# Performance work log

Measured on AMD Instinct MI355X. Metric: run time of the kernel, lower is better.

Reference implementation:

```python
import jax, jax.numpy as jnp
import numpy as np

IN_FEATURES = 4096
OUT_FEATURES = 4096
CODESZ = 8
CODEBOOK_SIZE = 256


def fwht(x):
    """Normalized fast Walsh-Hadamard transform over the last dim (power of 2).
    Equivalent to x @ (H / sqrt(n)); H symmetric so this serves both
    matmul_hadUt and matmul_hadU in the power-of-2 case (had=None, K=1)."""
    orig_shape = x.shape
    n = orig_shape[-1]
    x = x.reshape(-1, n)
    h = 2
    while h <= n:
        x = x.reshape(-1, n // h, 2, h // 2)
        a, b = x[..., 0, :], x[..., 1, :]
        x = jnp.stack([a + b, a - b], axis=-2)
        h *= 2
    x = x.reshape(orig_shape)
    return x * (1.0 / np.sqrt(n)).astype(np.float32)


def setup_inputs() -> dict:
    key = jax.random.key(0)
    k1, k2, k3, k4, k5, k6 = jax.random.split(key, 6)
    x = jax.random.normal(k1, (4, 2048, IN_FEATURES), dtype=jnp.float32)
    Qidxs = jax.random.randint(k2, (OUT_FEATURES, IN_FEATURES // CODESZ), 0, CODEBOOK_SIZE, dtype=jnp.int32)
    grid = jax.random.normal(k3, (CODEBOOK_SIZE, CODESZ), dtype=jnp.float32)
    SU = jax.random.uniform(k4, (IN_FEATURES,), dtype=jnp.float32)
    SV = jax.random.uniform(k5, (OUT_FEATURES,), dtype=jnp.float32)
    bias = jax.random.normal(k6, (OUT_FEATURES,), dtype=jnp.float32)
    return {"x": x, "Qidxs": Qidxs, "grid": grid, "SU": SU, "SV": SV, "bias": bias}


def reference(x, Qidxs, grid, SU, SV, bias):
    lead = x.shape[:-1]
    h = x.reshape(-1, IN_FEATURES)            # [T, in]
    h = h * SU                                 # scale by SU
    h = fwht(h)                                # matmul_hadUt (input rotation)
    # codebook dequant: gather code vectors and form W_hat [out, in]
    W_hat = grid[Qidxs].reshape(OUT_FEATURES, IN_FEATURES)
    y = h @ W_hat.T                            # [T, out]
    y = fwht(y)[:, :OUT_FEATURES]              # matmul_hadU (output rotation)
    y = y * SV
    y = y.reshape(*lead, OUT_FEATURES) + bias
    return y
```

## Files before the change

kernel.cpp:

```cpp
#include <hip/hip_runtime.h>

#define IN_F 4096
#define OUT_F 4096
#define NROWS 8192
#define BK 32
#define NT (IN_F / BK)

typedef __attribute__((ext_vector_type(4))) float f32x4;
typedef __attribute__((ext_vector_type(8))) short bf16x8;
typedef __attribute__((ext_vector_type(8))) unsigned short u16x8;

__device__ __forceinline__ unsigned short f2bf(float f) {
  union { float f; unsigned u; } x; x.f = f;
  unsigned r = x.u + 0x7FFFu + ((x.u >> 16) & 1u);
  return (unsigned short)(r >> 16);
}

__device__ __forceinline__ void gload_lds16(const unsigned short* g, unsigned short* l) {
  __builtin_amdgcn_global_load_lds((__attribute__((address_space(1))) void*)g,
                                   (__attribute__((address_space(3))) void*)l,
                                   16, 0, 0);
}

__device__ __forceinline__ void bfly16(float v[16]) {
#pragma unroll
  for (int s = 1; s < 16; s <<= 1) {
#pragma unroll
    for (int i = 0; i < 16; ++i) {
      if (!(i & s)) { float a = v[i], b = v[i + s]; v[i] = a + b; v[i + s] = a - b; }
    }
  }
}

__global__ __launch_bounds__(256) void dequant_kernel(const int* __restrict__ Q,
                                                      const float* __restrict__ grid,
                                                      unsigned short* __restrict__ Wb) {
  int g = blockIdx.x * 256 + threadIdx.x;
  int idx = Q[g];
  const f32x4* gp = (const f32x4*)(grid + idx * 8);
  f32x4 v0 = gp[0], v1 = gp[1];
  u16x8 o;
  o[0] = f2bf(v0[0]); o[1] = f2bf(v0[1]); o[2] = f2bf(v0[2]); o[3] = f2bf(v0[3]);
  o[4] = f2bf(v1[0]); o[5] = f2bf(v1[1]); o[6] = f2bf(v1[2]); o[7] = f2bf(v1[3]);
  *(u16x8*)(Wb + (size_t)g * 8) = o;
}

__global__ __launch_bounds__(256) void fwht1_kernel(const float* __restrict__ x,
                                                    const float* __restrict__ SU,
                                                    unsigned short* __restrict__ Hb) {
  __shared__ float buf[4096];
  int tid = threadIdx.x;
  size_t rbase = (size_t)blockIdx.x * IN_F;
  const f32x4* x4 = (const f32x4*)(x + rbase);
  const f32x4* su4 = (const f32x4*)SU;
  f32x4* b4 = (f32x4*)buf;
#pragma unroll
  for (int s = 0; s < 4; ++s) {
    int c = tid + 256 * s;
    f32x4 v = x4[c];
    f32x4 u = su4[c];
    v.x *= u.x; v.y *= u.y; v.z *= u.z; v.w *= u.w;
    b4[c] = v;
  }
  __syncthreads();
  float v[16];
  {
#pragma unroll
    for (int j = 0; j < 4; ++j) {
      f32x4 t4 = b4[tid * 4 + j];
      v[j*4+0] = t4.x; v[j*4+1] = t4.y; v[j*4+2] = t4.z; v[j*4+3] = t4.w;
    }
    bfly16(v);
#pragma unroll
    for (int j = 0; j < 4; ++j) {
      f32x4 t4; t4.x = v[j*4+0]; t4.y = v[j*4+1]; t4.z = v[j*4+2]; t4.w = v[j*4+3];
      b4[tid * 4 + j] = t4;
    }
  }
  __syncthreads();
  {
    int lo = tid & 15, hi = tid >> 4;
    int base = lo + (hi << 8);
#pragma unroll
    for (int j = 0; j < 16; ++j) v[j] = buf[base + (j << 4)];
    bfly16(v);
#pragma unroll
    for (int j = 0; j < 16; ++j) buf[base + (j << 4)] = v[j];
  }
  __syncthreads();
  {
#pragma unroll
    for (int j = 0; j < 16; ++j) v[j] = buf[tid + (j << 8)];
    bfly16(v);
#pragma unroll
    for (int j = 0; j < 16; ++j)
      Hb[rbase + tid + (j << 8)] = f2bf(v[j] * 0.015625f);
  }
}

__global__ __launch_bounds__(512) void gemm256_kernel(const unsigned short* __restrict__ Hb,
                                                      const unsigned short* __restrict__ Wb,
                                                      float* __restrict__ Y) {
  __shared__ unsigned short lds[4][2][256 * BK];
  const int tid = threadIdx.x;
  const int lane = tid & 63;
  const int wid = tid >> 6;
  const int wr = wid >> 2;
  const int wc = wid & 3;
  const int lrow = lane & 15;
  const int kgrp = lane >> 4;

  const int bid = blockIdx.x;
  const int swz = (bid & 7) * 64 + (bid >> 3);
  const int brow = (swz >> 4) << 8;
  const int bcol = (swz & 15) << 8;

  const int r0 = tid >> 2;
  const int sc = ((tid & 3) ^ ((r0 >> 1) & 3)) << 3;
  const unsigned short* AgR0 = Hb + (size_t)(brow + r0) * IN_F + sc;
  const unsigned short* AgR1 = Hb + (size_t)(brow + r0 + 128) * IN_F + sc;
  const unsigned short* BgR0 = Wb + (size_t)(bcol + r0) * IN_F + sc;
  const unsigned short* BgR1 = Wb + (size_t)(bcol + r0 + 128) * IN_F + sc;

#define STAGE(t) { \
  gload_lds16(AgR0 + (t) * BK, &lds[(t) & 3][0][tid * 8]); \
  gload_lds16(AgR1 + (t) * BK, &lds[(t) & 3][0][(tid + 512) * 8]); \
  gload_lds16(BgR0 + (t) * BK, &lds[(t) & 3][1][tid * 8]); \
  gload_lds16(BgR1 + (t) * BK, &lds[(t) & 3][1][(tid + 512) * 8]); }

  auto fragLd = [&](const unsigned short* base, int R) -> bf16x8 {
    return *(const bf16x8*)(base + R * BK + ((kgrp ^ ((R >> 1) & 3)) << 3));
  };

  const int ar = wr * 128 + lrow;
  const int br = wc * 64 + lrow;

#define READ_A(t, aS) { const unsigned short* As_ = &lds[(t) & 3][0][0]; \
  aS[0] = fragLd(As_, ar +   0); aS[1] = fragLd(As_, ar +  16); \
  aS[2] = fragLd(As_, ar +  32); aS[3] = fragLd(As_, ar +  48); \
  aS[4] = fragLd(As_, ar +  64); aS[5] = fragLd(As_, ar +  80); \
  aS[6] = fragLd(As_, ar +  96); aS[7] = fragLd(As_, ar + 112); }
#define READ_B(t) { const unsigned short* Bs_ = &lds[(t) & 3][1][0]; \
  b0 = fragLd(Bs_, br +  0); b1 = fragLd(Bs_, br + 16); \
  b2 = fragLd(Bs_, br + 32); b3 = fragLd(Bs_, br + 48); }

#define MM(i, A, B) acc[i] = __builtin_amdgcn_mfma_f32_16x16x32_bf16(A, B, acc[i], 0, 0, 0)
#define MMROW(m, aS) { \
  MM((m)*4+0, aS[m], b0); MM((m)*4+1, aS[m], b1); \
  MM((m)*4+2, aS[m], b2); MM((m)*4+3, aS[m], b3); }

#define TILE_BODY(t, aCur, aNxt) { \
  if ((t) + 3 <= NT) { asm volatile("s_waitcnt vmcnt(4)" ::: "memory"); } \
  else               { asm volatile("s_waitcnt vmcnt(0)" ::: "memory"); } \
  __builtin_amdgcn_s_barrier(); \
  if ((t) + 3 < NT) STAGE((t) + 3); \
  READ_B(t); \
  asm volatile("s_waitcnt lgkmcnt(0)" ::: "memory"); \
  __builtin_amdgcn_sched_barrier(0); \
  __builtin_amdgcn_s_setprio(1); \
  MMROW(0, aCur); MMROW(1, aCur); \
  __builtin_amdgcn_s_setprio(0); \
  if ((t) + 1 < NT) READ_A((t) + 1, aNxt); \
  __builtin_amdgcn_sched_barrier(0); \
  __builtin_amdgcn_s_setprio(1); \
  MMROW(2, aCur); MMROW(3, aCur); MMROW(4, aCur); MMROW(5, aCur); \
  MMROW(6, aCur); MMROW(7, aCur); \
  __builtin_amdgcn_s_setprio(0); }

  f32x4 acc[32] = {};
  bf16x8 aC[8], aN[8], b0, b1, b2, b3;

  STAGE(0); STAGE(1); STAGE(2);
  asm volatile("s_waitcnt vmcnt(4)" ::: "memory");
  __builtin_amdgcn_s_barrier();
  READ_A(0, aC);

  for (int t = 0; t < NT; t += 2) {
    TILE_BODY(t,     aC, aN);
    TILE_BODY(t + 1, aN, aC);
  }

#pragma unroll
  for (int mf = 0; mf < 8; ++mf) {
    int grow = brow + wr * 128 + mf * 16 + kgrp * 4;
    float* yp = Y + (size_t)grow * OUT_F + bcol + wc * 64 + lrow;
#pragma unroll
    for (int r = 0; r < 4; ++r)
#pragma unroll
      for (int nf = 0; nf < 4; ++nf)
        yp[(size_t)r * OUT_F + nf * 16] = acc[mf * 4 + nf][r];
  }
#undef STAGE
#undef READ_A
#undef READ_B
#undef MM
#undef MMROW
#undef TILE_BODY
}

__global__ __launch_bounds__(256) void fwht2_kernel(float* __restrict__ Y,
                                                    const float* __restrict__ SV,
                                                    const float* __restrict__ bias) {
  __shared__ float buf[4096];
  int tid = threadIdx.x;
  size_t rbase = (size_t)blockIdx.x * OUT_F;
  f32x4* y4 = (f32x4*)(Y + rbase);
  f32x4* b4 = (f32x4*)buf;
#pragma unroll
  for (int s = 0; s < 4; ++s) {
    int c = tid + 256 * s;
    b4[c] = y4[c];
  }
  __syncthreads();
  float v[16];
  {
#pragma unroll
    for (int j = 0; j < 4; ++j) {
      f32x4 t4 = b4[tid * 4 + j];
      v[j*4+0] = t4.x; v[j*4+1] = t4.y; v[j*4+2] = t4.z; v[j*4+3] = t4.w;
    }
    bfly16(v);
#pragma unroll
    for (int j = 0; j < 4; ++j) {
      f32x4 t4; t4.x = v[j*4+0]; t4.y = v[j*4+1]; t4.z = v[j*4+2]; t4.w = v[j*4+3];
      b4[tid * 4 + j] = t4;
    }
  }
  __syncthreads();
  {
    int lo = tid & 15, hi = tid >> 4;
    int base = lo + (hi << 8);
#pragma unroll
    for (int j = 0; j < 16; ++j) v[j] = buf[base + (j << 4)];
    bfly16(v);
#pragma unroll
    for (int j = 0; j < 16; ++j) buf[base + (j << 4)] = v[j];
  }
  __syncthreads();
  {
#pragma unroll
    for (int j = 0; j < 16; ++j) v[j] = buf[tid + (j << 8)];
    bfly16(v);
#pragma unroll
    for (int j = 0; j < 16; ++j) {
      int col = tid + (j << 8);
      Y[rbase + col] = v[j] * 0.015625f * SV[col] + bias[col];
    }
  }
}

extern "C" void kernel_launch(void* const* d_in, const int* in_sizes, int n_in,
                              void* d_out, int out_size, void* d_ws, size_t ws_size,
                              hipStream_t stream) {
  const float* x     = (const float*)d_in[0];
  const int*   Qidxs = (const int*)d_in[1];
  const float* grid  = (const float*)d_in[2];
  const float* SU    = (const float*)d_in[3];
  const float* SV    = (const float*)d_in[4];
  const float* bias  = (const float*)d_in[5];
  float* out = (float*)d_out;

  unsigned short* Wb = (unsigned short*)d_ws;
  unsigned short* Hb = Wb + (size_t)OUT_F * IN_F;

  hipLaunchKernelGGL(dequant_kernel, dim3((OUT_F * (IN_F / 8)) / 256), dim3(256), 0, stream,
                     Qidxs, grid, Wb);
  hipLaunchKernelGGL(fwht1_kernel, dim3(NROWS), dim3(256), 0, stream, x, SU, Hb);
  hipLaunchKernelGGL(gemm256_kernel, dim3((NROWS / 256) * (OUT_F / 256)), dim3(512), 0, stream,
                     Hb, Wb, out);
  hipLaunchKernelGGL(fwht2_kernel, dim3(NROWS), dim3(256), 0, stream, out, SV, bias);
}
```

Baseline: 330.8 us.

## Switch GEMM to 32x32x16 bf16 MFMA tiles and request two blocks per CU

Replaces the 16x16x32 MFMA fragment scheme with 32x32x16 bf16 MFMAs. Each wave tile becomes 4x2 32x32 accumulators, and the LDS fragment reads and the epilogue store mapping are rewritten to match. Larger MFMAs cut the instruction count and raise operand reuse per LDS read. Launch bounds now also ask for 2 blocks per CU, which limits registers per thread. LDS use is unchanged at 128 KB per block, so occupancy may not actually double.

```diff
diff --git a/kernel.cpp b/kernel.cpp
--- a/kernel.cpp
+++ b/kernel.cpp
@@ -7,6 +7,7 @@
 #define NT (IN_F / BK)
 
 typedef __attribute__((ext_vector_type(4))) float f32x4;
+typedef __attribute__((ext_vector_type(16))) float f32x16;
 typedef __attribute__((ext_vector_type(8))) short bf16x8;
 typedef __attribute__((ext_vector_type(8))) unsigned short u16x8;
 
@@ -98,17 +99,17 @@
   }
 }
 
-__global__ __launch_bounds__(512) void gemm256_kernel(const unsigned short* __restrict__ Hb,
-                                                      const unsigned short* __restrict__ Wb,
-                                                      float* __restrict__ Y) {
+__global__ __launch_bounds__(512, 2) void gemm256_kernel(const unsigned short* __restrict__ Hb,
+                                                         const unsigned short* __restrict__ Wb,
+                                                         float* __restrict__ Y) {
   __shared__ unsigned short lds[4][2][256 * BK];
   const int tid = threadIdx.x;
   const int lane = tid & 63;
   const int wid = tid >> 6;
   const int wr = wid >> 2;
   const int wc = wid & 3;
-  const int lrow = lane & 15;
-  const int kgrp = lane >> 4;
+  const int l31 = lane & 31;
+  const int hi5 = lane >> 5;
 
   const int bid = blockIdx.x;
   const int swz = (bid & 7) * 64 + (bid >> 3);
@@ -128,26 +129,25 @@
   gload_lds16(BgR0 + (t) * BK, &lds[(t) & 3][1][tid * 8]); \
   gload_lds16(BgR1 + (t) * BK, &lds[(t) & 3][1][(tid + 512) * 8]); }
 
-  auto fragLd = [&](const unsigned short* base, int R) -> bf16x8 {
-    return *(const bf16x8*)(base + R * BK + ((kgrp ^ ((R >> 1) & 3)) << 3));
+  auto fr32 = [&](const unsigned short* base, int Rblk, int kk) -> bf16x8 {
+    int row = Rblk + l31;
+    int slot = ((kk << 1) + hi5) ^ ((row >> 1) & 3);
+    return *(const bf16x8*)(base + row * BK + (slot << 3));
   };
 
-  const int ar = wr * 128 + lrow;
-  const int br = wc * 64 + lrow;
+  const int ar = wr * 128;
+  const int br = wc * 64;
 
 #define READ_A(t, aS) { const unsigned short* As_ = &lds[(t) & 3][0][0]; \
-  aS[0] = fragLd(As_, ar +   0); aS[1] = fragLd(As_, ar +  16); \
-  aS[2] = fragLd(As_, ar +  32); aS[3] = fragLd(As_, ar +  48); \
-  aS[4] = fragLd(As_, ar +  64); aS[5] = fragLd(As_, ar +  80); \
-  aS[6] = fragLd(As_, ar +  96); aS[7] = fragLd(As_, ar + 112); }
+  aS[0] = fr32(As_, ar +  0, 0); aS[1] = fr32(As_, ar +  0, 1); \
+  aS[2] = fr32(As_, ar + 32, 0); aS[3] = fr32(As_, ar + 32, 1); \
+  aS[4] = fr32(As_, ar + 64, 0); aS[5] = fr32(As_, ar + 64, 1); \
+  aS[6] = fr32(As_, ar + 96, 0); aS[7] = fr32(As_, ar + 96, 1); }
 #define READ_B(t) { const unsigned short* Bs_ = &lds[(t) & 3][1][0]; \
-  b0 = fragLd(Bs_, br +  0); b1 = fragLd(Bs_, br + 16); \
-  b2 = fragLd(Bs_, br + 32); b3 = fragLd(Bs_, br + 48); }
-
-#define MM(i, A, B) acc[i] = __builtin_amdgcn_mfma_f32_16x16x32_bf16(A, B, acc[i], 0, 0, 0)
-#define MMROW(m, aS) { \
-  MM((m)*4+0, aS[m], b0); MM((m)*4+1, aS[m], b1); \
-  MM((m)*4+2, aS[m], b2); MM((m)*4+3, aS[m], b3); }
+  b0 = fr32(Bs_, br +  0, 0); b1 = fr32(Bs_, br +  0, 1); \
+  b2 = fr32(Bs_, br + 32, 0); b3 = fr32(Bs_, br + 32, 1); }
+
+#define MM(f, A, B) acc[f] = __builtin_amdgcn_mfma_f32_32x32x16_bf16(A, B, acc[f], 0, 0, 0)
 
 #define TILE_BODY(t, aCur, aNxt) { \
   if ((t) + 3 <= NT) { asm volatile("s_waitcnt vmcnt(4)" ::: "memory"); } \
@@ -158,16 +158,21 @@
   asm volatile("s_waitcnt lgkmcnt(0)" ::: "memory"); \
   __builtin_amdgcn_sched_barrier(0); \
   __builtin_amdgcn_s_setprio(1); \
-  MMROW(0, aCur); MMROW(1, aCur); \
+  MM(0, aCur[0], b0); MM(1, aCur[0], b2); \
+  MM(2, aCur[2], b0); MM(3, aCur[2], b2); \
+  MM(4, aCur[4], b0); MM(5, aCur[4], b2); \
+  MM(6, aCur[6], b0); MM(7, aCur[6], b2); \
   __builtin_amdgcn_s_setprio(0); \
   if ((t) + 1 < NT) READ_A((t) + 1, aNxt); \
   __builtin_amdgcn_sched_barrier(0); \
   __builtin_amdgcn_s_setprio(1); \
-  MMROW(2, aCur); MMROW(3, aCur); MMROW(4, aCur); MMROW(5, aCur); \
-  MMROW(6, aCur); MMROW(7, aCur); \
+  MM(0, aCur[1], b1); MM(1, aCur[1], b3); \
+  MM(2, aCur[3], b1); MM(3, aCur[3], b3); \
+  MM(4, aCur[5], b1); MM(5, aCur[5], b3); \
+  MM(6, aCur[7], b1); MM(7, aCur[7], b3); \
   __builtin_amdgcn_s_setprio(0); }
 
-  f32x4 acc[32] = {};
+  f32x16 acc[8] = {};
   bf16x8 aC[8], aN[8], b0, b1, b2, b3;
 
   STAGE(0); STAGE(1); STAGE(2);
@@ -181,20 +186,22 @@
   }
 
 #pragma unroll
-  for (int mf = 0; mf < 8; ++mf) {
-    int grow = brow + wr * 128 + mf * 16 + kgrp * 4;
-    float* yp = Y + (size_t)grow * OUT_F + bcol + wc * 64 + lrow;
-#pragma unroll
-    for (int r = 0; r < 4; ++r)
-#pragma unroll
-      for (int nf = 0; nf < 4; ++nf)
-        yp[(size_t)r * OUT_F + nf * 16] = acc[mf * 4 + nf][r];
-  }
+  for (int mi = 0; mi < 4; ++mi)
+#pragma unroll
+    for (int ni = 0; ni < 2; ++ni) {
+      int f = mi * 2 + ni;
+      int gr = brow + wr * 128 + mi * 32 + 4 * hi5;
+      float* yp = Y + (size_t)gr * OUT_F + bcol + wc * 64 + ni * 32 + l31;
+#pragma unroll
+      for (int r = 0; r < 16; ++r) {
+        int rr = (r & 3) + 8 * (r >> 2);
+        yp[(size_t)rr * OUT_F] = acc[f][r];
+      }
+    }
 #undef STAGE
 #undef READ_A
 #undef READ_B
 #undef MM
-#undef MMROW
 #undef TILE_BODY
 }
 
```

Measured after the change: 357.5 us. 8.1% more time.

## Load GEMM A-operand fragments directly from global memory into registers, bypassing LDS

Applied to the files above, without the earlier changes.

The H operand no longer goes through LDS. Each wave now loads its A fragments straight from global memory into registers one K-tile ahead, and only the weight tiles stay in the 4-deep LDS ring. This removes the A LDS writes and reads, halves shared-memory use, and merges the MFMA rows into one block. In exchange, the four waves that share the same rows each fetch those A rows separately, the per-lane 16-byte row-strided loads are poorly coalesced, and only one tile of prefetch has to hide global latency.

```diff
diff --git a/kernel.cpp b/kernel.cpp
--- a/kernel.cpp
+++ b/kernel.cpp
@@ -101,7 +101,7 @@
 __global__ __launch_bounds__(512) void gemm256_kernel(const unsigned short* __restrict__ Hb,
                                                       const unsigned short* __restrict__ Wb,
                                                       float* __restrict__ Y) {
-  __shared__ unsigned short lds[4][2][256 * BK];
+  __shared__ unsigned short lds[4][256 * BK];
   const int tid = threadIdx.x;
   const int lane = tid & 63;
   const int wid = tid >> 6;
@@ -117,32 +117,29 @@
 
   const int r0 = tid >> 2;
   const int sc = ((tid & 3) ^ ((r0 >> 1) & 3)) << 3;
-  const unsigned short* AgR0 = Hb + (size_t)(brow + r0) * IN_F + sc;
-  const unsigned short* AgR1 = Hb + (size_t)(brow + r0 + 128) * IN_F + sc;
   const unsigned short* BgR0 = Wb + (size_t)(bcol + r0) * IN_F + sc;
   const unsigned short* BgR1 = Wb + (size_t)(bcol + r0 + 128) * IN_F + sc;
 
-#define STAGE(t) { \
-  gload_lds16(AgR0 + (t) * BK, &lds[(t) & 3][0][tid * 8]); \
-  gload_lds16(AgR1 + (t) * BK, &lds[(t) & 3][0][(tid + 512) * 8]); \
-  gload_lds16(BgR0 + (t) * BK, &lds[(t) & 3][1][tid * 8]); \
-  gload_lds16(BgR1 + (t) * BK, &lds[(t) & 3][1][(tid + 512) * 8]); }
+#define STAGE_B(t) { \
+  gload_lds16(BgR0 + (t) * BK, &lds[(t) & 3][tid * 8]); \
+  gload_lds16(BgR1 + (t) * BK, &lds[(t) & 3][(tid + 512) * 8]); }
 
   auto fragLd = [&](const unsigned short* base, int R) -> bf16x8 {
     return *(const bf16x8*)(base + R * BK + ((kgrp ^ ((R >> 1) & 3)) << 3));
   };
 
-  const int ar = wr * 128 + lrow;
   const int br = wc * 64 + lrow;
 
-#define READ_A(t, aS) { const unsigned short* As_ = &lds[(t) & 3][0][0]; \
-  aS[0] = fragLd(As_, ar +   0); aS[1] = fragLd(As_, ar +  16); \
-  aS[2] = fragLd(As_, ar +  32); aS[3] = fragLd(As_, ar +  48); \
-  aS[4] = fragLd(As_, ar +  64); aS[5] = fragLd(As_, ar +  80); \
-  aS[6] = fragLd(As_, ar +  96); aS[7] = fragLd(As_, ar + 112); }
-#define READ_B(t) { const unsigned short* Bs_ = &lds[(t) & 3][1][0]; \
+#define READ_B(t) { const unsigned short* Bs_ = &lds[(t) & 3][0]; \
   b0 = fragLd(Bs_, br +  0); b1 = fragLd(Bs_, br + 16); \
   b2 = fragLd(Bs_, br + 32); b3 = fragLd(Bs_, br + 48); }
+
+  const unsigned short* pA = Hb + (size_t)(brow + wr * 128 + lrow) * IN_F + kgrp * 8;
+
+#define LOAD_A(t, aS) { \
+  _Pragma("unroll") \
+  for (int m = 0; m < 8; ++m) \
+    aS[m] = *(const bf16x8*)(pA + (size_t)m * 16 * IN_F + (t) * BK); }
 
 #define MM(i, A, B) acc[i] = __builtin_amdgcn_mfma_f32_16x16x32_bf16(A, B, acc[i], 0, 0, 0)
 #define MMROW(m, aS) { \
@@ -150,30 +147,26 @@
   MM((m)*4+2, aS[m], b2); MM((m)*4+3, aS[m], b3); }
 
 #define TILE_BODY(t, aCur, aNxt) { \
-  if ((t) + 3 <= NT) { asm volatile("s_waitcnt vmcnt(4)" ::: "memory"); } \
-  else               { asm volatile("s_waitcnt vmcnt(0)" ::: "memory"); } \
+  if ((t) + 2 < NT) { asm volatile("s_waitcnt vmcnt(2)" ::: "memory"); } \
+  else              { asm volatile("s_waitcnt vmcnt(0)" ::: "memory"); } \
   __builtin_amdgcn_s_barrier(); \
-  if ((t) + 3 < NT) STAGE((t) + 3); \
   READ_B(t); \
+  if ((t) + 1 < NT) LOAD_A((t) + 1, aNxt); \
+  if ((t) + 3 < NT) STAGE_B((t) + 3); \
   asm volatile("s_waitcnt lgkmcnt(0)" ::: "memory"); \
   __builtin_amdgcn_sched_barrier(0); \
   __builtin_amdgcn_s_setprio(1); \
-  MMROW(0, aCur); MMROW(1, aCur); \
-  __builtin_amdgcn_s_setprio(0); \
-  if ((t) + 1 < NT) READ_A((t) + 1, aNxt); \
-  __builtin_amdgcn_sched_barrier(0); \
-  __builtin_amdgcn_s_setprio(1); \
-  MMROW(2, aCur); MMROW(3, aCur); MMROW(4, aCur); MMROW(5, aCur); \
-  MMROW(6, aCur); MMROW(7, aCur); \
+  MMROW(0, aCur); MMROW(1, aCur); MMROW(2, aCur); MMROW(3, aCur); \
+  MMROW(4, aCur); MMROW(5, aCur); MMROW(6, aCur); MMROW(7, aCur); \
   __builtin_amdgcn_s_setprio(0); }
 
   f32x4 acc[32] = {};
   bf16x8 aC[8], aN[8], b0, b1, b2, b3;
 
-  STAGE(0); STAGE(1); STAGE(2);
-  asm volatile("s_waitcnt vmcnt(4)" ::: "memory");
+  STAGE_B(0); STAGE_B(1); STAGE_B(2);
+  LOAD_A(0, aC);
+  asm volatile("s_waitcnt vmcnt(0)" ::: "memory");
   __builtin_amdgcn_s_barrier();
-  READ_A(0, aC);
 
   for (int t = 0; t < NT; t += 2) {
     TILE_BODY(t,     aC, aN);
@@ -190,9 +183,9 @@
       for (int nf = 0; nf < 4; ++nf)
         yp[(size_t)r * OUT_F + nf * 16] = acc[mf * 4 + nf][r];
   }
-#undef STAGE
-#undef READ_A
+#undef STAGE_B
 #undef READ_B
+#undef LOAD_A
 #undef MM
 #undef MMROW
 #undef TILE_BODY
```

Result: slower. 667.4 us (+101.8%).
